# Kernel optimization log

Hardware: AMD Instinct MI355X
Metric: run time of the kernel (lower is better)

The kernel has to match this reference:

```python
import jax, jax.numpy as jnp
import numpy as np

B, T, A, H, L = 8, 100, 64, 512, 3


def setup_inputs() -> dict:
    key = jax.random.key(0)
    ks = jax.random.split(key, 6)
    s = 1.0 / np.sqrt(H)  # PyTorch GRU init range
    x = jax.random.normal(ks[0], (B, T, A, H), jnp.float32)
    valid = jax.random.randint(ks[1], (B, T, A), 0, 2) > 0
    w_ih = jax.random.uniform(ks[2], (L, 3 * H, H), jnp.float32, -s, s)
    w_hh = jax.random.uniform(ks[3], (L, 3 * H, H), jnp.float32, -s, s)
    b_ih = jax.random.uniform(ks[4], (L, 3 * H), jnp.float32, -s, s)
    b_hh = jax.random.uniform(ks[5], (L, 3 * H), jnp.float32, -s, s)
    return {"x": x, "valid": valid, "w_ih": w_ih, "w_hh": w_hh, "b_ih": b_ih, "b_hh": b_hh}


def reference(x, valid, w_ih, w_hh, b_ih, b_hh):
    # x: [B,T,A,H], valid: [B,T,A]; multi-layer GRU over time with per-step
    # zeroing of hidden state and output where the agent is invalid.
    Bx, Tx, Ax, Hx = x.shape
    Lx = w_ih.shape[0]
    xs = jnp.transpose(x, (1, 0, 2, 3)).reshape(Tx, Bx * Ax, Hx)          # [T, BA, H]
    inv = jnp.transpose(~valid, (1, 0, 2)).reshape(Tx, Bx * Ax, 1)        # [T, BA, 1]
    h0 = jnp.zeros((Lx, Bx * Ax, Hx), x.dtype)

    def step(h, inp_t):
        xt, inv_t = inp_t                      # xt: [BA,H], inv_t: [BA,1]
        layer_in = xt
        hs = []
        for l in range(Lx):                    # small fixed layer loop
            gi = layer_in @ w_ih[l].T + b_ih[l]   # [BA, 3H]
            gh = h[l] @ w_hh[l].T + b_hh[l]       # [BA, 3H]
            i_r, i_z, i_n = jnp.split(gi, 3, axis=-1)
            h_r, h_z, h_n = jnp.split(gh, 3, axis=-1)
            r = jax.nn.sigmoid(i_r + h_r)
            z = jax.nn.sigmoid(i_z + h_z)
            n = jnp.tanh(i_n + r * h_n)
            hl = (1.0 - z) * n + z * h[l]
            hs.append(hl)
            layer_in = hl
        h_new = jnp.where(inv_t, 0.0, jnp.stack(hs))  # mask all layers' state
        y = jnp.where(inv_t, 0.0, layer_in)           # masked top-layer output
        return h_new, y

    _, ys = jax.lax.scan(step, h0, (xs, inv))         # ys: [T, BA, H]
    x1 = jnp.transpose(ys.reshape(Tx, Bx, Ax, Hx), (1, 0, 2, 3))  # [B,T,A,H]
    return x1
```

## Files before the change

### kernel.cpp

```cpp
#include <hip/hip_runtime.h>

#define Tc 100
#define Hc 512
#define Lc 3
#define H3c 1536
#define HLAY (Hc*Hc)
#define HSLOT (Lc*HLAY)
#define HLPAR (6*256*512)

typedef short bf16x8 __attribute__((ext_vector_type(8)));
typedef float f32x4 __attribute__((ext_vector_type(4)));

__device__ __forceinline__ unsigned short f2bf(float f) {
  unsigned int u = __float_as_uint(f);
  u += 0x7FFFu + ((u >> 16) & 1u);
  return (unsigned short)(u >> 16);
}

__global__ __launch_bounds__(256) void conv_bf16(const float* __restrict__ src,
                                                 unsigned short* __restrict__ dst,
                                                 int n4) {
  int i = blockIdx.x * 256 + threadIdx.x;
  if (i >= n4) return;
  f32x4 v = *(const f32x4*)(src + (size_t)i * 4);
  ushort4 o;
  o.x = f2bf(v[0]); o.y = f2bf(v[1]); o.z = f2bf(v[2]); o.w = f2bf(v[3]);
  *(ushort4*)(dst + (size_t)i * 4) = o;
}

__device__ __forceinline__ void waitg(const int* slots, int tgt, int lane) {
  const int* p = slots + (lane & 31);
  int it = 0;
  for (;;) {
    int v;
    asm volatile("global_load_dword %0, %1, off sc0 sc1\n\ts_waitcnt vmcnt(0)"
                 : "=v"(v) : "v"(p) : "memory");
    if (__all(v >= tgt)) break;
    __builtin_amdgcn_s_sleep(1);
    if (++it > 4000000) break;
  }
}

#define LOADC(dst, ptr) \
  asm volatile("global_load_dwordx4 %0, %1, off sc0 sc1" : "=v"(dst) : "v"(ptr))
#define LOADL(dst, ptr) \
  asm volatile("global_load_dwordx4 %0, %1, off sc0" : "=v"(dst) : "v"(ptr))
#define LOADN(dst, ptr) \
  asm volatile("global_load_dwordx4 %0, %1, off" : "=v"(dst) : "v"(ptr))
#define STORE_H2(ptr, v32) \
  asm volatile("global_store_short %0, %1, off sc0 sc1" :: "v"(ptr), "v"(v32))
#define STORE_HL(ptr, v32) \
  asm volatile("global_store_short %0, %1, off sc0" :: "v"(ptr), "v"(v32))
#define STORE_D(ptr, v32) \
  asm volatile("global_store_dword %0, %1, off sc0 sc1" :: "v"(ptr), "v"(v32))
#define WAITV(n) do { asm volatile("s_waitcnt vmcnt(" #n ")" ::: "memory"); \
                      __builtin_amdgcn_sched_barrier(0); } while (0)
#define MM(a, b, c) c = __builtin_amdgcn_mfma_f32_16x16x32_bf16(a, b, c, 0, 0, 0)

__global__ __launch_bounds__(256, 1) void gru_persist13(
    const float* __restrict__ x,
    const short* __restrict__ xb,
    const short* __restrict__ wbih,
    const short* __restrict__ wbhh,
    const float* __restrict__ bih,
    const float* __restrict__ bhh,
    short* hb,
    short* hbl,
    const int* __restrict__ valid,
    float* __restrict__ y,
    int* done) {
  __shared__ char wlds[98304];

  const int bid = blockIdx.x;
  const int gi = bid & 7;
  if (gi >= 6) return;
  const int cb = bid >> 3;
  const int l = gi >> 1;
  const int rb = gi & 1;
  const int c0 = cb * 16;
  const int R0 = rb * 256;

  const int tid = threadIdx.x;
  const int w = tid >> 6;
  const int lane = tid & 63;
  const int lrow = lane & 15;
  const int kgrp = lane >> 4;

  const short* wih_l = wbih + (size_t)l * H3c * Hc;
  const short* whh_l = wbhh + (size_t)l * H3c * Hc;

#pragma unroll
  for (int j4 = 0; j4 < 24; ++j4) {
    int j = j4 * 4 + w;
    int m = j >> 4, ks = j & 15;
    int g = (m < 3) ? m : m - 3;
    int n = g * Hc + c0 + lrow;
    const short* src = ((m < 3) ? wih_l : whh_l) + (size_t)n * Hc + ks * 32 + kgrp * 8;
    *(bf16x8*)(wlds + (size_t)j * 1024 + lane * 16) = *(const bf16x8*)src;
  }
  __syncthreads();

  const char* wl = wlds + (lane << 4);

  const float* bihl = bih + l * H3c;
  const float* bhhl = bhh + l * H3c;
  const int c = c0 + lrow;
  const float bi0 = bihl[c], bi1 = bihl[Hc + c], bi2 = bihl[2 * Hc + c];
  const float bh0 = bhhl[c], bh1 = bhhl[Hc + c], bh2 = bhhl[2 * Hc + c];

  f32x4 hreg[4];
#pragma unroll
  for (int rf = 0; rf < 4; ++rf) hreg[rf] = f32x4{0.f, 0.f, 0.f, 0.f};

  WAITV(0);

  for (int t = 0; t < Tc; ++t) {
    if (w == 1 && t > 0)           waitg(done + gi * 32, t, lane);
    if (w == 2 && l < 2 && t >= 2) waitg(done + ((l + 1) * 2 + rb) * 32, t - 1, lane);
    __syncthreads();

    const int par = t & 1;

    const short* pHL[4];
    const short* pA[4] = {nullptr, nullptr, nullptr, nullptr};
    const float* pXf[4] = {x, x, x, x};
    {
      const short* hprevL = hbl + (size_t)(1 - par) * HLPAR + (size_t)gi * 131072;
#pragma unroll
      for (int rf = 0; rf < 4; ++rf) {
        int rowl = w * 64 + rf * 16 + lrow;
        pHL[rf] = hprevL + (size_t)rowl * Hc;
        int row = R0 + rowl;
        if (l > 0) {
          pA[rf] = hb + (size_t)par * HSLOT + (size_t)(l - 1) * HLAY + (size_t)row * Hc;
        } else {
          int bb = row >> 6, aa = row & 63;
          size_t rofs = ((size_t)bb * Tc + t) * 64 + aa;
          if (xb) pA[rf] = xb + rofs * Hc;
          pXf[rf] = x + rofs * Hc;
        }
      }
    }

    f32x4 acc[6][4];
#pragma unroll
    for (int m = 0; m < 6; ++m)
#pragma unroll
      for (int rf = 0; rf < 4; ++rf) acc[m][rf] = f32x4{0.f, 0.f, 0.f, 0.f};

#define ISSUE_HL(H_, g2)                                                           \
      { _Pragma("unroll") for (int rf = 0; rf < 4; ++rf)                           \
          _Pragma("unroll") for (int k2 = 0; k2 < 2; ++k2) {                       \
            const int ke = ((g2) * 2 + k2) * 32 + (kgrp << 3);                     \
            LOADL(H_[rf][k2], pHL[rf] + ke);                                       \
          } }
#define ISSUE_AC(A_, g2)                                                           \
      { _Pragma("unroll") for (int rf = 0; rf < 4; ++rf)                           \
          _Pragma("unroll") for (int k2 = 0; k2 < 2; ++k2) {                       \
            const int ke = ((g2) * 2 + k2) * 32 + (kgrp << 3);                     \
            LOADC(A_[rf][k2], pA[rf] + ke);                                        \
          } }
#define ISSUE_AN(A_, g2)                                                           \
      { _Pragma("unroll") for (int rf = 0; rf < 4; ++rf)                           \
          _Pragma("unroll") for (int k2 = 0; k2 < 2; ++k2) {                       \
            const int ke = ((g2) * 2 + k2) * 32 + (kgrp << 3);                     \
            LOADN(A_[rf][k2], pA[rf] + ke);                                        \
          } }
#define CONSUME_H(H_, g2)                                                          \
      { _Pragma("unroll") for (int k2 = 0; k2 < 2; ++k2) {                         \
          const int ks = (g2) * 2 + k2;                                            \
          bf16x8 Bg3 = *(const bf16x8*)(wl + ((3 * 16 + ks) << 10));               \
          bf16x8 Bg4 = *(const bf16x8*)(wl + ((4 * 16 + ks) << 10));               \
          bf16x8 Bg5 = *(const bf16x8*)(wl + ((5 * 16 + ks) << 10));               \
          _Pragma("unroll") for (int rf = 0; rf < 4; ++rf) {                       \
            MM(H_[rf][k2], Bg3, acc[3][rf]);                                       \
            MM(H_[rf][k2], Bg4, acc[4][rf]);                                       \
            MM(H_[rf][k2], Bg5, acc[5][rf]);                                       \
          } } }
#define CONSUME_A(A_, g2)                                                          \
      { _Pragma("unroll") for (int k2 = 0; k2 < 2; ++k2) {                         \
          const int ks = (g2) * 2 + k2;                                            \
          bf16x8 Bg0 = *(const bf16x8*)(wl + ((0 * 16 + ks) << 10));               \
          bf16x8 Bg1 = *(const bf16x8*)(wl + ((1 * 16 + ks) << 10));               \
          bf16x8 Bg2 = *(const bf16x8*)(wl + ((2 * 16 + ks) << 10));               \
          _Pragma("unroll") for (int rf = 0; rf < 4; ++rf) {                       \
            MM(A_[rf][k2], Bg0, acc[0][rf]);                                       \
            MM(A_[rf][k2], Bg1, acc[1][rf]);                                       \
            MM(A_[rf][k2], Bg2, acc[2][rf]);                                       \
          } } }
#define PASS(ISS, CONS)                                                            \
      { bf16x8 Ra[4][2], Rb[4][2];                                                 \
        ISS(Ra, 0);                                                                \
        _Pragma("unroll") for (int g2 = 0; g2 < 8; g2 += 2) {                      \
          ISS(Rb, g2 + 1);                                                         \
          WAITV(8);                                                                \
          CONS(Ra, g2);                                                            \
          if (g2 + 2 < 8) {                                                        \
            ISS(Ra, g2 + 2);                                                       \
            WAITV(8);                                                              \
          } else {                                                                 \
            WAITV(0);                                                              \
          }                                                                        \
          CONS(Rb, g2 + 1);                                                        \
        } }

    __builtin_amdgcn_sched_barrier(0);
    if (t > 0) {
      PASS(ISSUE_HL, CONSUME_H)
    }
    if (l > 0) {
      if (w == 0) waitg(done + ((l - 1) * 2 + rb) * 32, t + 1, lane);
      __syncthreads();
      __builtin_amdgcn_sched_barrier(0);
      PASS(ISSUE_AC, CONSUME_A)
    } else if (xb) {
      PASS(ISSUE_AN, CONSUME_A)
    } else {
#pragma unroll
      for (int g2 = 0; g2 < 8; ++g2) {
        bf16x8 Aa[4][2];
#pragma unroll
        for (int rf = 0; rf < 4; ++rf)
#pragma unroll
          for (int k2 = 0; k2 < 2; ++k2) {
            const int ks = g2 * 2 + k2;
            const float* _px = pXf[rf] + ks * 32 + (kgrp << 3);
            f32x4 v0 = *(const f32x4*)_px;
            f32x4 v1 = *(const f32x4*)(_px + 4);
            bf16x8 t_;
#pragma unroll
            for (int e = 0; e < 4; ++e) {
              t_[e] = (short)f2bf(v0[e]); t_[4 + e] = (short)f2bf(v1[e]);
            }
            Aa[rf][k2] = t_;
          }
        WAITV(0);
        CONSUME_A(Aa, g2);
      }
    }
    __builtin_amdgcn_sched_barrier(0);

    short* hout = hb + (size_t)par * HSLOT + (size_t)l * HLAY;
    short* houtL = hbl + (size_t)par * HLPAR + (size_t)gi * 131072;
#pragma unroll
    for (int rf = 0; rf < 4; ++rf) {
#pragma unroll
      for (int rr = 0; rr < 4; ++rr) {
        int mloc = w * 64 + rf * 16 + kgrp * 4 + rr;
        int rowg = R0 + mloc;
        int bb = rowg >> 6, aa = rowg & 63;
        size_t vofs = ((size_t)bb * Tc + t) * 64 + aa;
        int vld = valid[vofs];
        float ir = acc[0][rf][rr] + bi0;
        float iz = acc[1][rf][rr] + bi1;
        float in_ = acc[2][rf][rr] + bi2;
        float hr = acc[3][rf][rr] + bh0;
        float hz = acc[4][rf][rr] + bh1;
        float hn = acc[5][rf][rr] + bh2;
        float rg = 1.0f / (1.0f + __expf(-(ir + hr)));
        float zg = 1.0f / (1.0f + __expf(-(iz + hz)));
        float ng = tanhf(in_ + rg * hn);
        float hnew = (1.0f - zg) * ng + zg * hreg[rf][rr];
        if (!vld) hnew = 0.0f;
        hreg[rf][rr] = hnew;
        int hv = (int)f2bf(hnew);
        STORE_HL(houtL + (size_t)mloc * Hc + c, hv);
        if (l < 2) STORE_H2(hout + (size_t)rowg * Hc + c, hv);
        else       y[vofs * Hc + c] = hnew;
      }
    }

    asm volatile("s_waitcnt vmcnt(0)" ::: "memory");
    __syncthreads();
    if (tid == 0) {
      int v = t + 1;
      STORE_D(done + gi * 32 + cb, v);
    }
    WAITV(0);
  }
}

extern "C" void kernel_launch(void* const* d_in, const int* in_sizes, int n_in,
                              void* d_out, int out_size, void* d_ws, size_t ws_size,
                              hipStream_t stream) {
  const float* x = (const float*)d_in[0];
  const int* valid = (const int*)d_in[1];
  const float* w_ih = (const float*)d_in[2];
  const float* w_hh = (const float*)d_in[3];
  const float* b_ih = (const float*)d_in[4];
  const float* b_hh = (const float*)d_in[5];
  float* y = (float*)d_out;

  char* ws = (char*)d_ws;
  const size_t welems = (size_t)Lc * H3c * Hc;
  unsigned short* wbih = (unsigned short*)ws;
  unsigned short* wbhh = (unsigned short*)(ws + welems * 2);
  short* hb = (short*)(ws + welems * 4);
  const size_t hb_bytes = (size_t)2 * HSLOT * 2;
  int* done = (int*)(ws + welems * 4 + hb_bytes);
  const size_t flags_bytes = 4800;
  const size_t hbl_off = welems * 4 + hb_bytes + flags_bytes;
  const size_t hbl_bytes = (size_t)2 * HLPAR * 2;
  short* hbl = (short*)(ws + hbl_off);
  const size_t xb_off = hbl_off + hbl_bytes;
  const size_t xelems = (size_t)8 * Tc * 64 * Hc;
  const bool big = ws_size >= xb_off + xelems * 2;
  unsigned short* xbf = big ? (unsigned short*)(ws + xb_off) : nullptr;

  int n4w = (int)(welems / 4);
  conv_bf16<<<(n4w + 255) / 256, 256, 0, stream>>>(w_ih, wbih, n4w);
  conv_bf16<<<(n4w + 255) / 256, 256, 0, stream>>>(w_hh, wbhh, n4w);
  if (big) {
    int n4x = (int)(xelems / 4);
    conv_bf16<<<(n4x + 255) / 256, 256, 0, stream>>>(x, xbf, n4x);
  }
  (void)hipMemsetAsync(hb, 0, hb_bytes + flags_bytes, stream);

  gru_persist13<<<256, 256, 0, stream>>>(x, (const short*)xbf,
                                         (const short*)wbih, (const short*)wbhh,
                                         b_ih, b_hh, hb, hbl, valid, y, done);
}
```

Measured before the change: 2.538 ms.

## Split per-block GRU rows across 16 waves instead of 4, shrinking per-wave register tiles

Blocks now launch with 1024 threads (16 waves), and each wave handles 16 rows instead of 64. Accumulators, loads and hidden registers per wave shrink by 4x. The intent is more waves to hide global load latency and MFMA dependency chains inside the latency-bound persistent recurrence, and each block's share of each step is done sooner. The spin-wait uses a longer sleep per poll, with a lower iteration cap. That reduces polling traffic but can add wake-up latency. Each wave now re-reads the same LDS weights for fewer rows, and the 1024-thread __syncthreads barriers cost more.

```diff
diff --git a/kernel.cpp b/kernel.cpp
--- a/kernel.cpp
+++ b/kernel.cpp
@@ -36,8 +36,8 @@
     asm volatile("global_load_dword %0, %1, off sc0 sc1\n\ts_waitcnt vmcnt(0)"
                  : "=v"(v) : "v"(p) : "memory");
     if (__all(v >= tgt)) break;
-    __builtin_amdgcn_s_sleep(1);
-    if (++it > 4000000) break;
+    __builtin_amdgcn_s_sleep(8);
+    if (++it > 1000000) break;
   }
 }
 
@@ -57,7 +57,7 @@
                       __builtin_amdgcn_sched_barrier(0); } while (0)
 #define MM(a, b, c) c = __builtin_amdgcn_mfma_f32_16x16x32_bf16(a, b, c, 0, 0, 0)
 
-__global__ __launch_bounds__(256, 1) void gru_persist13(
+__global__ __launch_bounds__(1024, 4) void gru_persist14(
     const float* __restrict__ x,
     const short* __restrict__ xb,
     const short* __restrict__ wbih,
@@ -90,8 +90,8 @@
   const short* whh_l = wbhh + (size_t)l * H3c * Hc;
 
 #pragma unroll
-  for (int j4 = 0; j4 < 24; ++j4) {
-    int j = j4 * 4 + w;
+  for (int it = 0; it < 6; ++it) {
+    int j = it * 16 + w;
     int m = j >> 4, ks = j & 15;
     int g = (m < 3) ? m : m - 3;
     int n = g * Hc + c0 + lrow;
@@ -108,9 +108,7 @@
   const float bi0 = bihl[c], bi1 = bihl[Hc + c], bi2 = bihl[2 * Hc + c];
   const float bh0 = bhhl[c], bh1 = bhhl[Hc + c], bh2 = bhhl[2 * Hc + c];
 
-  f32x4 hreg[4];
-#pragma unroll
-  for (int rf = 0; rf < 4; ++rf) hreg[rf] = f32x4{0.f, 0.f, 0.f, 0.f};
+  f32x4 hreg = f32x4{0.f, 0.f, 0.f, 0.f};
 
   WAITV(0);
 
@@ -120,122 +118,82 @@
     __syncthreads();
 
     const int par = t & 1;
-
-    const short* pHL[4];
-    const short* pA[4] = {nullptr, nullptr, nullptr, nullptr};
-    const float* pXf[4] = {x, x, x, x};
+    const int rowl = w * 16 + lrow;
+
+    const short* pHL = hbl + (size_t)(1 - par) * HLPAR + (size_t)gi * 131072
+                       + (size_t)rowl * Hc;
+    const short* pA = nullptr;
+    const float* pXf = x;
     {
-      const short* hprevL = hbl + (size_t)(1 - par) * HLPAR + (size_t)gi * 131072;
-#pragma unroll
-      for (int rf = 0; rf < 4; ++rf) {
-        int rowl = w * 64 + rf * 16 + lrow;
-        pHL[rf] = hprevL + (size_t)rowl * Hc;
-        int row = R0 + rowl;
-        if (l > 0) {
-          pA[rf] = hb + (size_t)par * HSLOT + (size_t)(l - 1) * HLAY + (size_t)row * Hc;
-        } else {
-          int bb = row >> 6, aa = row & 63;
-          size_t rofs = ((size_t)bb * Tc + t) * 64 + aa;
-          if (xb) pA[rf] = xb + rofs * Hc;
-          pXf[rf] = x + rofs * Hc;
-        }
+      int row = R0 + rowl;
+      if (l > 0) {
+        pA = hb + (size_t)par * HSLOT + (size_t)(l - 1) * HLAY + (size_t)row * Hc;
+      } else {
+        int bb = row >> 6, aa = row & 63;
+        size_t rofs = ((size_t)bb * Tc + t) * 64 + aa;
+        if (xb) pA = xb + rofs * Hc;
+        pXf = x + rofs * Hc;
       }
     }
 
-    f32x4 acc[6][4];
-#pragma unroll
-    for (int m = 0; m < 6; ++m)
-#pragma unroll
-      for (int rf = 0; rf < 4; ++rf) acc[m][rf] = f32x4{0.f, 0.f, 0.f, 0.f};
-
-#define ISSUE_HL(H_, g2)                                                           \
-      { _Pragma("unroll") for (int rf = 0; rf < 4; ++rf)                           \
-          _Pragma("unroll") for (int k2 = 0; k2 < 2; ++k2) {                       \
-            const int ke = ((g2) * 2 + k2) * 32 + (kgrp << 3);                     \
-            LOADL(H_[rf][k2], pHL[rf] + ke);                                       \
-          } }
-#define ISSUE_AC(A_, g2)                                                           \
-      { _Pragma("unroll") for (int rf = 0; rf < 4; ++rf)                           \
-          _Pragma("unroll") for (int k2 = 0; k2 < 2; ++k2) {                       \
-            const int ke = ((g2) * 2 + k2) * 32 + (kgrp << 3);                     \
-            LOADC(A_[rf][k2], pA[rf] + ke);                                        \
-          } }
-#define ISSUE_AN(A_, g2)                                                           \
-      { _Pragma("unroll") for (int rf = 0; rf < 4; ++rf)                           \
-          _Pragma("unroll") for (int k2 = 0; k2 < 2; ++k2) {                       \
-            const int ke = ((g2) * 2 + k2) * 32 + (kgrp << 3);                     \
-            LOADN(A_[rf][k2], pA[rf] + ke);                                        \
-          } }
-#define CONSUME_H(H_, g2)                                                          \
-      { _Pragma("unroll") for (int k2 = 0; k2 < 2; ++k2) {                         \
-          const int ks = (g2) * 2 + k2;                                            \
-          bf16x8 Bg3 = *(const bf16x8*)(wl + ((3 * 16 + ks) << 10));               \
-          bf16x8 Bg4 = *(const bf16x8*)(wl + ((4 * 16 + ks) << 10));               \
-          bf16x8 Bg5 = *(const bf16x8*)(wl + ((5 * 16 + ks) << 10));               \
-          _Pragma("unroll") for (int rf = 0; rf < 4; ++rf) {                       \
-            MM(H_[rf][k2], Bg3, acc[3][rf]);                                       \
-            MM(H_[rf][k2], Bg4, acc[4][rf]);                                       \
-            MM(H_[rf][k2], Bg5, acc[5][rf]);                                       \
-          } } }
-#define CONSUME_A(A_, g2)                                                          \
-      { _Pragma("unroll") for (int k2 = 0; k2 < 2; ++k2) {                         \
-          const int ks = (g2) * 2 + k2;                                            \
-          bf16x8 Bg0 = *(const bf16x8*)(wl + ((0 * 16 + ks) << 10));               \
-          bf16x8 Bg1 = *(const bf16x8*)(wl + ((1 * 16 + ks) << 10));               \
-          bf16x8 Bg2 = *(const bf16x8*)(wl + ((2 * 16 + ks) << 10));               \
-          _Pragma("unroll") for (int rf = 0; rf < 4; ++rf) {                       \
-            MM(A_[rf][k2], Bg0, acc[0][rf]);                                       \
-            MM(A_[rf][k2], Bg1, acc[1][rf]);                                       \
-            MM(A_[rf][k2], Bg2, acc[2][rf]);                                       \
-          } } }
-#define PASS(ISS, CONS)                                                            \
-      { bf16x8 Ra[4][2], Rb[4][2];                                                 \
-        ISS(Ra, 0);                                                                \
-        _Pragma("unroll") for (int g2 = 0; g2 < 8; g2 += 2) {                      \
-          ISS(Rb, g2 + 1);                                                         \
-          WAITV(8);                                                                \
-          CONS(Ra, g2);                                                            \
-          if (g2 + 2 < 8) {                                                        \
-            ISS(Ra, g2 + 2);                                                       \
-            WAITV(8);                                                              \
-          } else {                                                                 \
-            WAITV(0);                                                              \
-          }                                                                        \
-          CONS(Rb, g2 + 1);                                                        \
+    f32x4 acc[6];
+#pragma unroll
+    for (int m = 0; m < 6; ++m) acc[m] = f32x4{0.f, 0.f, 0.f, 0.f};
+
+#define ISS4(LOADM, P_, R_, b)                                                     \
+      { _Pragma("unroll") for (int q = 0; q < 4; ++q) {                            \
+          const int ks = (b) + q;                                                  \
+          LOADM(R_[ks & 7], P_ + ks * 32 + (kgrp << 3));                           \
         } }
+#define CON4(R_, b, M0)                                                            \
+      { _Pragma("unroll") for (int q = 0; q < 4; ++q) {                            \
+          const int ks = (b) + q;                                                  \
+          bf16x8 B0 = *(const bf16x8*)(wl + (((M0) * 16 + ks) << 10));             \
+          bf16x8 B1 = *(const bf16x8*)(wl + ((((M0) + 1) * 16 + ks) << 10));       \
+          bf16x8 B2 = *(const bf16x8*)(wl + ((((M0) + 2) * 16 + ks) << 10));       \
+          MM(R_[ks & 7], B0, acc[(M0)]);                                           \
+          MM(R_[ks & 7], B1, acc[(M0) + 1]);                                       \
+          MM(R_[ks & 7], B2, acc[(M0) + 2]);                                       \
+        } }
+#define PASS(LOADM, P_, M0)                                                        \
+      { bf16x8 R_[8];                                                              \
+        ISS4(LOADM, P_, R_, 0);  ISS4(LOADM, P_, R_, 4);                           \
+        WAITV(4); CON4(R_, 0, M0);                                                 \
+        ISS4(LOADM, P_, R_, 8);                                                    \
+        WAITV(4); CON4(R_, 4, M0);                                                 \
+        ISS4(LOADM, P_, R_, 12);                                                   \
+        WAITV(4); CON4(R_, 8, M0);                                                 \
+        WAITV(0); CON4(R_, 12, M0);                                                \
+      }
 
     __builtin_amdgcn_sched_barrier(0);
     if (t > 0) {
-      PASS(ISSUE_HL, CONSUME_H)
+      PASS(LOADL, pHL, 3)
     }
     if (l > 0) {
       if (w == 0) waitg(done + ((l - 1) * 2 + rb) * 32, t + 1, lane);
       __syncthreads();
       __builtin_amdgcn_sched_barrier(0);
-      PASS(ISSUE_AC, CONSUME_A)
+      PASS(LOADC, pA, 0)
     } else if (xb) {
-      PASS(ISSUE_AN, CONSUME_A)
+      PASS(LOADN, pA, 0)
     } else {
 #pragma unroll
-      for (int g2 = 0; g2 < 8; ++g2) {
-        bf16x8 Aa[4][2];
-#pragma unroll
-        for (int rf = 0; rf < 4; ++rf)
-#pragma unroll
-          for (int k2 = 0; k2 < 2; ++k2) {
-            const int ks = g2 * 2 + k2;
-            const float* _px = pXf[rf] + ks * 32 + (kgrp << 3);
-            f32x4 v0 = *(const f32x4*)_px;
-            f32x4 v1 = *(const f32x4*)(_px + 4);
-            bf16x8 t_;
-#pragma unroll
-            for (int e = 0; e < 4; ++e) {
-              t_[e] = (short)f2bf(v0[e]); t_[4 + e] = (short)f2bf(v1[e]);
-            }
-            Aa[rf][k2] = t_;
-          }
-        WAITV(0);
-        CONSUME_A(Aa, g2);
+      for (int ks = 0; ks < 16; ++ks) {
+        const float* _px = pXf + ks * 32 + (kgrp << 3);
+        f32x4 v0 = *(const f32x4*)_px;
+        f32x4 v1 = *(const f32x4*)(_px + 4);
+        bf16x8 t_;
+#pragma unroll
+        for (int e = 0; e < 4; ++e) {
+          t_[e] = (short)f2bf(v0[e]); t_[4 + e] = (short)f2bf(v1[e]);
+        }
+        bf16x8 B0 = *(const bf16x8*)(wl + ((0 * 16 + ks) << 10));
+        bf16x8 B1 = *(const bf16x8*)(wl + ((1 * 16 + ks) << 10));
+        bf16x8 B2 = *(const bf16x8*)(wl + ((2 * 16 + ks) << 10));
+        MM(t_, B0, acc[0]);
+        MM(t_, B1, acc[1]);
+        MM(t_, B2, acc[2]);
       }
     }
     __builtin_amdgcn_sched_barrier(0);
@@ -243,31 +201,28 @@
     short* hout = hb + (size_t)par * HSLOT + (size_t)l * HLAY;
     short* houtL = hbl + (size_t)par * HLPAR + (size_t)gi * 131072;
 #pragma unroll
-    for (int rf = 0; rf < 4; ++rf) {
-#pragma unroll
-      for (int rr = 0; rr < 4; ++rr) {
-        int mloc = w * 64 + rf * 16 + kgrp * 4 + rr;
-        int rowg = R0 + mloc;
-        int bb = rowg >> 6, aa = rowg & 63;
-        size_t vofs = ((size_t)bb * Tc + t) * 64 + aa;
-        int vld = valid[vofs];
-        float ir = acc[0][rf][rr] + bi0;
-        float iz = acc[1][rf][rr] + bi1;
-        float in_ = acc[2][rf][rr] + bi2;
-        float hr = acc[3][rf][rr] + bh0;
-        float hz = acc[4][rf][rr] + bh1;
-        float hn = acc[5][rf][rr] + bh2;
-        float rg = 1.0f / (1.0f + __expf(-(ir + hr)));
-        float zg = 1.0f / (1.0f + __expf(-(iz + hz)));
-        float ng = tanhf(in_ + rg * hn);
-        float hnew = (1.0f - zg) * ng + zg * hreg[rf][rr];
-        if (!vld) hnew = 0.0f;
-        hreg[rf][rr] = hnew;
-        int hv = (int)f2bf(hnew);
-        STORE_HL(houtL + (size_t)mloc * Hc + c, hv);
-        if (l < 2) STORE_H2(hout + (size_t)rowg * Hc + c, hv);
-        else       y[vofs * Hc + c] = hnew;
-      }
+    for (int rr = 0; rr < 4; ++rr) {
+      int mloc = w * 16 + kgrp * 4 + rr;
+      int rowg = R0 + mloc;
+      int bb = rowg >> 6, aa = rowg & 63;
+      size_t vofs = ((size_t)bb * Tc + t) * 64 + aa;
+      int vld = valid[vofs];
+      float ir = acc[0][rr] + bi0;
+      float iz = acc[1][rr] + bi1;
+      float in_ = acc[2][rr] + bi2;
+      float hr = acc[3][rr] + bh0;
+      float hz = acc[4][rr] + bh1;
+      float hn = acc[5][rr] + bh2;
+      float rg = 1.0f / (1.0f + __expf(-(ir + hr)));
+      float zg = 1.0f / (1.0f + __expf(-(iz + hz)));
+      float ng = tanhf(in_ + rg * hn);
+      float hnew = (1.0f - zg) * ng + zg * hreg[rr];
+      if (!vld) hnew = 0.0f;
+      hreg[rr] = hnew;
+      int hv = (int)f2bf(hnew);
+      STORE_HL(houtL + (size_t)mloc * Hc + c, hv);
+      if (l < 2) STORE_H2(hout + (size_t)rowg * Hc + c, hv);
+      else       y[vofs * Hc + c] = hnew;
     }
 
     asm volatile("s_waitcnt vmcnt(0)" ::: "memory");
@@ -316,7 +271,7 @@
   }
   (void)hipMemsetAsync(hb, 0, hb_bytes + flags_bytes, stream);
 
-  gru_persist13<<<256, 256, 0, stream>>>(x, (const short*)xbf,
-                                         (const short*)wbih, (const short*)wbhh,
-                                         b_ih, b_hh, hb, hbl, valid, y, done);
-}
+  gru_persist14<<<256, 1024, 0, stream>>>(x, (const short*)xbf,
+                                          (const short*)wbih, (const short*)wbhh,
+                                          b_ih, b_hh, hb, hbl, valid, y, done);
+}
```

After: 2.049 ms. 19.3% less time.
